# Optimization experiments

Hardware: AMD Instinct MI355X
Metric: run time of the kernel (lower is better)

Reference implementation:

```python
import jax, jax.numpy as jnp
import numpy as np

B, S, D, H = 2, 2048, 1024, 16
DK = D // H

def setup_inputs() -> dict:
    key = jax.random.key(0)
    ks = jax.random.split(key, 11)
    scale = 0.02
    inp = {
        "Q": jax.random.normal(ks[0], (B, S, D), jnp.float32),
        "K": jax.random.normal(ks[1], (B, S, D), jnp.float32),
        "V": jax.random.normal(ks[2], (B, S, D), jnp.float32),
        "mask": jnp.ones((B, S), jnp.int32),
        "Wq": jax.random.normal(ks[3], (D, D), jnp.float32) * scale,
        "bq": jnp.zeros((D,), jnp.float32),
        "Wk": jax.random.normal(ks[4], (D, D), jnp.float32) * scale,
        "bk": jnp.zeros((D,), jnp.float32),
        "Wv": jax.random.normal(ks[5], (D, D), jnp.float32) * scale,
        "bv": jnp.zeros((D,), jnp.float32),
        "Wo": jax.random.normal(ks[6], (D, D), jnp.float32) * scale,
        "bo": jnp.zeros((D,), jnp.float32),
    }
    return inp

def _split_heads(x):
    # [B,S,D] -> [B,H,S,DK]
    return x.reshape(B, S, H, DK).transpose(0, 2, 1, 3)

def reference(Q, K, V, mask, Wq, bq, Wk, bk, Wv, bv, Wo, bo):
    q = _split_heads(Q @ Wq.T + bq)
    k = _split_heads(K @ Wk.T + bk)
    v = _split_heads(V @ Wv.T + bv)
    scores = jnp.einsum("bhqd,bhkd->bhqk", q, k) / jnp.sqrt(jnp.float32(DK))
    # 2D padding mask -> [B,1,1,S], mask==0 positions set to -inf
    m = mask[:, None, None, :]
    scores = jnp.where(m == 0, -jnp.inf, scores)
    attn_weights = jax.nn.softmax(scores, axis=-1)  # [B,H,S,S]
    attn_output = jnp.einsum("bhqk,bhkd->bhqd", attn_weights, v)
    attn_output = attn_output.transpose(0, 2, 1, 3).reshape(B, S, D)
    output = attn_output @ Wo.T + bo
    return (output, attn_weights)
```

## Files before the change

### kernel.cpp

```cpp
#include <hip/hip_runtime.h>
#include <stdint.h>

#define DEVINL __device__ __forceinline__

typedef float  f32x4  __attribute__((ext_vector_type(4)));
typedef float  f32x16 __attribute__((ext_vector_type(16)));
typedef short  s16x8  __attribute__((ext_vector_type(8)));
typedef unsigned short u16x4 __attribute__((ext_vector_type(4)));
typedef unsigned short u16x8 __attribute__((ext_vector_type(8)));

static constexpr int S = 2048, D = 1024, H = 16;
static constexpr size_t OUT0 = (size_t)2 * S * D;

DEVINL unsigned short f2bf(float f) {
  union { float f; unsigned u; } v; v.f = f;
  unsigned r = v.u + 0x7FFFu + ((v.u >> 16) & 1u);
  return (unsigned short)(r >> 16);
}

DEVINL unsigned cvt_pk_bf16(float lo, float hi) {
  unsigned r;
  asm("v_cvt_pk_bf16_f32 %0, %1, %2" : "=v"(r) : "v"(lo), "v"(hi));
  return r;
}

DEVINL void perm32swap(unsigned& a, unsigned& b) {
#if __has_builtin(__builtin_amdgcn_permlane32_swap)
  auto r = __builtin_amdgcn_permlane32_swap(a, b, false, false);
  a = r[0]; b = r[1];
#else
  asm volatile("v_permlane32_swap_b32 %0, %1" : "+v"(a), "+v"(b));
#endif
}

DEVINL void gload_lds16(const void* g, void* l) {
  __builtin_amdgcn_global_load_lds(
      (const __attribute__((address_space(1))) unsigned int*)g,
      (__attribute__((address_space(3))) unsigned int*)l, 16, 0, 0);
}

DEVINL void cvt_body(const float* __restrict__ src, unsigned short* __restrict__ dst, int i) {
  const f32x4* s4 = (const f32x4*)src;
  f32x4 a = s4[i * 2], b = s4[i * 2 + 1];
  u16x8 o;
  o[0] = f2bf(a[0]); o[1] = f2bf(a[1]); o[2] = f2bf(a[2]); o[3] = f2bf(a[3]);
  o[4] = f2bf(b[0]); o[5] = f2bf(b[1]); o[6] = f2bf(b[2]); o[7] = f2bf(b[3]);
  ((u16x8*)dst)[i] = o;
}

__global__ __launch_bounds__(256) void k_cvt_all(
    const float* __restrict__ Q, const float* __restrict__ K, const float* __restrict__ V,
    const float* __restrict__ Wq, const float* __restrict__ Wk,
    const float* __restrict__ Wv, const float* __restrict__ Wo,
    unsigned short* __restrict__ Xq, unsigned short* __restrict__ Xk,
    unsigned short* __restrict__ Xv,
    unsigned short* __restrict__ WQ, unsigned short* __restrict__ WK,
    unsigned short* __restrict__ WV, unsigned short* __restrict__ WO) {
  int i = blockIdx.x;
  const float* src; unsigned short* dst; int item;
  if (i < 6144) {
    int z = i >> 11;
    item = (i & 2047) * 256 + threadIdx.x;
    src = z == 0 ? Q : z == 1 ? K : V;
    dst = z == 0 ? Xq : z == 1 ? Xk : Xv;
  } else {
    int j = i - 6144, z = j >> 9;
    item = (j & 511) * 256 + threadIdx.x;
    src = z == 0 ? Wq : z == 1 ? Wk : z == 2 ? Wv : Wo;
    dst = z == 0 ? WQ : z == 1 ? WK : z == 2 ? WV : WO;
  }
  cvt_body(src, dst, item);
}

template <int MODE>
DEVINL void gemm_tile(const unsigned short* __restrict__ A,
                      const unsigned short* __restrict__ Bw,
                      const float* __restrict__ bias, void* __restrict__ Cout,
                      int tileM, int tileN, float scl, char* smem) {
  unsigned short* As = (unsigned short*)smem;
  unsigned short* Bs = (unsigned short*)(smem + 8192);
  const int tid = threadIdx.x;
  const int lane = tid & 63, wave = tid >> 6;
  const int wr = wave >> 1, wc = wave & 1;
  const int l15 = lane & 15, l16 = lane >> 4;
  f32x4 acc[4][4] = {};
  for (int k0 = 0; k0 < 1024; k0 += 32) {
#pragma unroll
    for (int p = 0; p < 2; ++p) {
      int c = tid + p * 256;
      int row = c >> 2, col = (c & 3) * 8;
      gload_lds16(A + (((size_t)(tileM + row)) << 10) + k0 + col, &As[c * 8]);
      gload_lds16(Bw + (((size_t)(tileN + row)) << 10) + k0 + col, &Bs[c * 8]);
    }
    __syncthreads();
    s16x8 af[4], bf[4];
#pragma unroll
    for (int i = 0; i < 4; ++i)
      af[i] = *(const s16x8*)&As[(wr * 64 + i * 16 + l15) * 32 + l16 * 8];
#pragma unroll
    for (int i = 0; i < 4; ++i)
      bf[i] = *(const s16x8*)&Bs[(wc * 64 + i * 16 + l15) * 32 + l16 * 8];
#pragma unroll
    for (int i = 0; i < 4; ++i)
#pragma unroll
      for (int j = 0; j < 4; ++j)
        acc[i][j] = __builtin_amdgcn_mfma_f32_16x16x32_bf16(af[i], bf[j], acc[i][j], 0, 0, 0);
    __syncthreads();
  }

  if (MODE == 2) {
    unsigned short* T = (unsigned short*)smem;
#pragma unroll
    for (int i = 0; i < 4; ++i)
#pragma unroll
      for (int j = 0; j < 4; ++j) {
        int n = wc * 64 + j * 16 + l15;
        float bv = bias[tileN + n];
        int m0 = wr * 64 + i * 16 + l16 * 4;
        u16x4 o;
#pragma unroll
        for (int r = 0; r < 4; ++r) o[r] = f2bf(acc[i][j][r] + bv);
        *(u16x4*)((char*)T + n * 256 + ((m0 * 2) ^ ((n & 15) << 4))) = o;
      }
    __syncthreads();
    {
      int n = tid >> 1, mh = tid & 1;
      int d = (tileN + n) & 63, h_ = (tileN + n) >> 6;
      int b_ = tileM >> 11;
      int kt_ = (((tileM & 2047) + mh * 64) >> 6);
      unsigned short* dst = (unsigned short*)Cout + (size_t)(b_ * H + h_) * S * 64 +
                            (size_t)kt_ * 4096 + d * 64;
#pragma unroll
      for (int k = 0; k < 8; ++k) {
        int mc = mh * 64 + k * 8;
        u16x8 v = *(const u16x8*)((const char*)T + n * 256 + ((mc * 2) ^ ((n & 15) << 4)));
        *(u16x8*)(dst + k * 8) = v;
      }
    }
  } else {
#pragma unroll
    for (int i = 0; i < 4; ++i) {
#pragma unroll
      for (int j = 0; j < 4; ++j) {
        int n = tileN + wc * 64 + j * 16 + l15;
        float bv = bias[n];
#pragma unroll
        for (int r = 0; r < 4; ++r) {
          int m = tileM + wr * 64 + i * 16 + l16 * 4 + r;
          float v = (acc[i][j][r] + bv) * scl;
          if (MODE == 0) {
            int b_ = m >> 11, s_ = m & 2047, h_ = n >> 6, d_ = n & 63;
            ((unsigned short*)Cout)[(((size_t)(b_ * H + h_) * S) + s_) * 64 + d_] = f2bf(v);
          } else {
            ((float*)Cout)[(size_t)m * 1024 + n] = v;
          }
        }
      }
    }
  }
}

__global__ __launch_bounds__(256) void k_gemm_qkv(
    const unsigned short* __restrict__ Xq, const unsigned short* __restrict__ Xk,
    const unsigned short* __restrict__ Xv,
    const unsigned short* __restrict__ Wq, const unsigned short* __restrict__ Wk,
    const unsigned short* __restrict__ Wv,
    const float* __restrict__ bq, const float* __restrict__ bk, const float* __restrict__ bv,
    unsigned short* __restrict__ oq, unsigned short* __restrict__ ok,
    unsigned short* __restrict__ vt2) {
  __shared__ alignas(16) char smem[32768];
  int flat = (blockIdx.z * 32 + blockIdx.y) * 8 + blockIdx.x;
  int swz = (flat & 7) * 96 + (flat >> 3);
  int z = swz >> 8;
  int rem = swz & 255;
  int ty = rem >> 3, tx = rem & 7;
  if (z == 2) {
    gemm_tile<2>(Xv, Wv, bv, vt2, ty * 128, tx * 128, 1.0f, smem);
  } else {
    const unsigned short* A = z == 0 ? Xq : Xk;
    const unsigned short* W = z == 0 ? Wq : Wk;
    const float* bias = z == 0 ? bq : bk;
    unsigned short* o = z == 0 ? oq : ok;
    gemm_tile<0>(A, W, bias, o, ty * 128, tx * 128, z == 0 ? 0.125f : 1.0f, smem);
  }
}

__global__ __launch_bounds__(256) void k_gemm_out(const unsigned short* __restrict__ A,
                                                  const unsigned short* __restrict__ W,
                                                  const float* __restrict__ bias,
                                                  float* __restrict__ Cout) {
  __shared__ alignas(16) char smem[16384];
  int flat = blockIdx.y * 8 + blockIdx.x;
  int swz = (flat & 7) * 32 + (flat >> 3);
  int ty = swz >> 3, tx = swz & 7;
  gemm_tile<1>(A, W, bias, Cout, ty * 128, tx * 128, 1.0f, smem);
}

__global__ __launch_bounds__(256) void k_attn_fused(const unsigned short* __restrict__ qw,
                                                    const unsigned short* __restrict__ kw,
                                                    const unsigned short* __restrict__ vt2,
                                                    const int* __restrict__ mask,
                                                    unsigned short* __restrict__ aout,
                                                    float* __restrict__ attw) {
  __shared__ alignas(16) char lds[33536];
  unsigned short* Ks = (unsigned short*)lds;
  unsigned short* Vs = (unsigned short*)(lds + 16384);
  float* lsumW = (float*)(lds + 32768);
  float* lsumT = (float*)(lds + 33280);
  float* nl2lW = (float*)(lds + 33408);
  const float LOG2E = 1.44269504f;

  int flat = blockIdx.y * 64 + blockIdx.x;
  int swzb = (flat & 7) * 256 + (flat >> 3);
  const int bh = swzb >> 6, b = bh >> 4, h = bh & 15;
  const int q0 = (swzb & 63) * 32;
  const int tid = threadIdx.x;
  const int lane = tid & 63, w = tid >> 6;
  const int l31 = lane & 31, hi = lane >> 5;

  const unsigned short* kw_bh = kw + (size_t)bh * S * 64;
  const unsigned short* vt_bh = vt2 + (size_t)bh * S * 64;
  const int* mrow = mask + b * S;

  s16x8 qf[4];
  const unsigned short* qbase = qw + ((size_t)bh * S + q0 + l31) * 64 + hi * 8;
#pragma unroll
  for (int kc = 0; kc < 4; ++kc) qf[kc] = *(const s16x8*)(qbase + kc * 16);

  f32x16 oT0 = {}, oT1 = {};
  float lsum = 0.f;
  const int swv = (l31 & 15) << 4;

  for (int t = 0; t < 16; ++t) {
#pragma unroll
    for (int p = 0; p < 4; ++p) {
      int c = tid + p * 256, row = c >> 3, cc = (c & 7) ^ (row & 7);
      gload_lds16(kw_bh + ((size_t)(t * 128 + row)) * 64 + cc * 8, Ks + c * 8);
    }
#pragma unroll
    for (int p = 0; p < 4; ++p) {
      int c = tid + p * 256, row = c >> 4, c16 = (c & 15) ^ (row & 15);
      gload_lds16(vt_bh + (size_t)(t * 2 + (c16 >> 3)) * 4096 + row * 64 + (c16 & 7) * 8,
                  Vs + c * 8);
    }
    __syncthreads();

    const int krow = w * 32 + l31;
    f32x16 sT = {};
#pragma unroll
    for (int kc = 0; kc < 4; ++kc) {
      s16x8 ka = *(const s16x8*)((const char*)Ks + krow * 128 +
                                 ((kc * 32 + hi * 16) ^ ((krow & 7) << 4)));
      sT = __builtin_amdgcn_mfma_f32_32x32x16_bf16(ka, qf[kc], sT, 0, 0, 0);
    }

    int base = t * 128 + w * 32 + 4 * hi;
    int m[16];
    *(int4*)&m[0]  = *(const int4*)&mrow[base];
    *(int4*)&m[4]  = *(const int4*)&mrow[base + 8];
    *(int4*)&m[8]  = *(const int4*)&mrow[base + 16];
    *(int4*)&m[12] = *(const int4*)&mrow[base + 24];

    float e[16];
#pragma unroll
    for (int r = 0; r < 16; ++r) {
      e[r] = m[r] ? exp2f(sT[r] * LOG2E) : 0.f;
      lsum += e[r];
    }

    unsigned x0 = cvt_pk_bf16(e[0], e[1]),   x1 = cvt_pk_bf16(e[2], e[3]);
    unsigned x2 = cvt_pk_bf16(e[4], e[5]),   x3 = cvt_pk_bf16(e[6], e[7]);
    unsigned x4 = cvt_pk_bf16(e[8], e[9]),   x5 = cvt_pk_bf16(e[10], e[11]);
    unsigned x6 = cvt_pk_bf16(e[12], e[13]), x7 = cvt_pk_bf16(e[14], e[15]);
    perm32swap(x0, x2); perm32swap(x1, x3);
    perm32swap(x4, x6); perm32swap(x5, x7);
    union { unsigned u[4]; s16x8 v; } p0u, p1u;
    p0u.u[0] = x0; p0u.u[1] = x1; p0u.u[2] = x2; p0u.u[3] = x3;
    p1u.u[0] = x4; p1u.u[1] = x5; p1u.u[2] = x6; p1u.u[3] = x7;

    const int ko0 = w * 64 + hi * 16, ko1 = w * 64 + 32 + hi * 16;
    const char* Vr0 = (const char*)Vs + l31 * 256;
    const char* Vr1 = (const char*)Vs + (32 + l31) * 256;
    s16x8 va;
    va = *(const s16x8*)(Vr0 + (ko0 ^ swv));
    oT0 = __builtin_amdgcn_mfma_f32_32x32x16_bf16(va, p0u.v, oT0, 0, 0, 0);
    va = *(const s16x8*)(Vr0 + (ko1 ^ swv));
    oT0 = __builtin_amdgcn_mfma_f32_32x32x16_bf16(va, p1u.v, oT0, 0, 0, 0);
    va = *(const s16x8*)(Vr1 + (ko0 ^ swv));
    oT1 = __builtin_amdgcn_mfma_f32_32x32x16_bf16(va, p0u.v, oT1, 0, 0, 0);
    va = *(const s16x8*)(Vr1 + (ko1 ^ swv));
    oT1 = __builtin_amdgcn_mfma_f32_32x32x16_bf16(va, p1u.v, oT1, 0, 0, 0);

    __syncthreads();
  }

  lsum += __shfl_xor(lsum, 32);
  if (hi == 0) lsumW[w * 32 + l31] = lsum;

  {
    char* orow = (char*)lds + w * 8192 + l31 * 256;
#pragma unroll
    for (int rg = 0; rg < 4; ++rg) {
      f32x4 c0, c1;
#pragma unroll
      for (int j = 0; j < 4; ++j) { c0[j] = oT0[rg * 4 + j]; c1[j] = oT1[rg * 4 + j]; }
      *(f32x4*)(orow + ((rg * 32 + hi * 16) ^ swv)) = c0;
      *(f32x4*)(orow + ((128 + rg * 32 + hi * 16) ^ swv)) = c1;
    }
  }
  __syncthreads();

  if (tid < 32) {
    float tot = lsumW[tid] + lsumW[32 + tid] + lsumW[64 + tid] + lsumW[96 + tid];
    lsumT[tid] = tot;
    nl2lW[tid] = __log2f(tot);
  }
  __syncthreads();

  {
    int q = tid >> 3, dg = tid & 7;
    float inv = 1.f / lsumT[q];
    int sq = (q & 15) << 4;
    float s[8] = {};
#pragma unroll
    for (int w4 = 0; w4 < 4; ++w4) {
      const char* prow = (const char*)lds + w4 * 8192 + q * 256;
      f32x4 a = *(const f32x4*)(prow + ((dg * 32) ^ sq));
      f32x4 bb = *(const f32x4*)(prow + ((dg * 32 + 16) ^ sq));
#pragma unroll
      for (int j = 0; j < 4; ++j) { s[j] += a[j]; s[4 + j] += bb[j]; }
    }
    u16x8 ob;
#pragma unroll
    for (int j = 0; j < 8; ++j) ob[j] = f2bf(s[j] * inv);
    *(u16x8*)&aout[((size_t)b * S + q0 + q) * D + h * 64 + dg * 8] = ob;
  }

  float nl2l[16];
#pragma unroll
  for (int r = 0; r < 16; ++r) nl2l[r] = nl2lW[(r & 3) + 8 * (r >> 2) + 4 * hi];

  for (int it = 0; it < 16; ++it) {
    int key0 = it * 128 + w * 32;
    const unsigned short* kbase = kw_bh + (size_t)(key0 + l31) * 64 + hi * 8;
    s16x8 kb[4];
#pragma unroll
    for (int kc = 0; kc < 4; ++kc) kb[kc] = *(const s16x8*)(kbase + kc * 16);
    f32x16 dacc = {};
#pragma unroll
    for (int kc = 0; kc < 4; ++kc)
      dacc = __builtin_amdgcn_mfma_f32_32x32x16_bf16(qf[kc], kb[kc], dacc, 0, 0, 0);

    int key = key0 + l31;
    int mk = mrow[key];
    float* obase = attw + ((size_t)bh * S + q0) * S + key;
#pragma unroll
    for (int r = 0; r < 16; ++r) {
      int row = (r & 3) + 8 * (r >> 2) + 4 * hi;
      float wv = mk ? exp2f(dacc[r] * LOG2E - nl2l[r]) : 0.f;
      __builtin_nontemporal_store(wv, obase + (size_t)row * S);
    }
  }
}

extern "C" void kernel_launch(void* const* d_in, const int* in_sizes, int n_in,
                              void* d_out, int out_size, void* d_ws, size_t ws_size,
                              hipStream_t stream) {
  (void)in_sizes; (void)n_in; (void)out_size; (void)ws_size;
  const float* Q  = (const float*)d_in[0];
  const float* K  = (const float*)d_in[1];
  const float* V  = (const float*)d_in[2];
  const int* mask = (const int*)d_in[3];
  const float* Wq = (const float*)d_in[4];
  const float* bq = (const float*)d_in[5];
  const float* Wk = (const float*)d_in[6];
  const float* bk = (const float*)d_in[7];
  const float* Wv = (const float*)d_in[8];
  const float* bv = (const float*)d_in[9];
  const float* Wo = (const float*)d_in[10];
  const float* bo = (const float*)d_in[11];

  char* ws = (char*)d_ws;
  unsigned short* Xbf  = (unsigned short*)(ws + 0);
  unsigned short* Wbf  = (unsigned short*)(ws + 25165824);
  unsigned short* qws  = (unsigned short*)(ws + 33554432);
  unsigned short* kws  = (unsigned short*)(ws + 41943040);
  unsigned short* vt2  = (unsigned short*)(ws + 50331648);
  unsigned short* aoutb= (unsigned short*)(ws + 8388608);
  float* out0 = (float*)d_out;
  float* attw = (float*)d_out + OUT0;

  k_cvt_all<<<dim3(8192), dim3(256), 0, stream>>>(
      Q, K, V, Wq, Wk, Wv, Wo,
      Xbf, Xbf + 4194304, Xbf + 8388608,
      Wbf, Wbf + 1048576, Wbf + 2097152, Wbf + 3145728);

  k_gemm_qkv<<<dim3(8, 32, 3), dim3(256), 0, stream>>>(
      Xbf, Xbf + 4194304, Xbf + 8388608,
      Wbf, Wbf + 1048576, Wbf + 2097152,
      bq, bk, bv, qws, kws, vt2);

  k_attn_fused<<<dim3(64, 32), dim3(256), 0, stream>>>(qws, kws, vt2, mask, aoutb, attw);

  k_gemm_out<<<dim3(8, 32), dim3(256), 0, stream>>>(aoutb, Wbf + 3145728, bo, out0);
}
```

Baseline: 241.7 us.

## Double-buffer K/V tiles and process 64 queries per attention block

The attention kernel now handles 64 queries per block (two query groups of two waves each, each wave covering 32 keys) instead of 32 queries with four waves over 128 keys. K and V tiles of 64 keys are double-buffered in LDS so the next tile's global-to-LDS load is issued before computing on the current one, removing one barrier-exposed load stall per iteration. Each K/V tile is reused by twice as many queries, halving K/V traffic per query, but the grid is halved to 1024 blocks and the reduction/epilogue indexing is rewritten.

```diff
diff --git a/kernel.cpp b/kernel.cpp
--- a/kernel.cpp
+++ b/kernel.cpp
@@ -202,59 +202,67 @@
                                                     const int* __restrict__ mask,
                                                     unsigned short* __restrict__ aout,
                                                     float* __restrict__ attw) {
-  __shared__ alignas(16) char lds[33536];
-  unsigned short* Ks = (unsigned short*)lds;
-  unsigned short* Vs = (unsigned short*)(lds + 16384);
+  __shared__ alignas(16) char lds[33792];
   float* lsumW = (float*)(lds + 32768);
   float* lsumT = (float*)(lds + 33280);
-  float* nl2lW = (float*)(lds + 33408);
+  float* nl2lW = (float*)(lds + 33536);
   const float LOG2E = 1.44269504f;
 
-  int flat = blockIdx.y * 64 + blockIdx.x;
-  int swzb = (flat & 7) * 256 + (flat >> 3);
-  const int bh = swzb >> 6, b = bh >> 4, h = bh & 15;
-  const int q0 = (swzb & 63) * 32;
+  int flat = blockIdx.y * 32 + blockIdx.x;
+  int swzb = (flat & 7) * 128 + (flat >> 3);
+  const int bh = swzb >> 5, b = bh >> 4, h = bh & 15;
+  const int q0 = (swzb & 31) * 64;
   const int tid = threadIdx.x;
   const int lane = tid & 63, w = tid >> 6;
   const int l31 = lane & 31, hi = lane >> 5;
+  const int qg = w >> 1, kb = w & 1;
 
   const unsigned short* kw_bh = kw + (size_t)bh * S * 64;
   const unsigned short* vt_bh = vt2 + (size_t)bh * S * 64;
   const int* mrow = mask + b * S;
 
   s16x8 qf[4];
-  const unsigned short* qbase = qw + ((size_t)bh * S + q0 + l31) * 64 + hi * 8;
+  const unsigned short* qbase = qw + ((size_t)bh * S + q0 + qg * 32 + l31) * 64 + hi * 8;
 #pragma unroll
   for (int kc = 0; kc < 4; ++kc) qf[kc] = *(const s16x8*)(qbase + kc * 16);
 
   f32x16 oT0 = {}, oT1 = {};
   float lsum = 0.f;
-  const int swv = (l31 & 15) << 4;
-
-  for (int t = 0; t < 16; ++t) {
-#pragma unroll
-    for (int p = 0; p < 4; ++p) {
-      int c = tid + p * 256, row = c >> 3, cc = (c & 7) ^ (row & 7);
-      gload_lds16(kw_bh + ((size_t)(t * 128 + row)) * 64 + cc * 8, Ks + c * 8);
-    }
-#pragma unroll
-    for (int p = 0; p < 4; ++p) {
-      int c = tid + p * 256, row = c >> 4, c16 = (c & 15) ^ (row & 15);
-      gload_lds16(vt_bh + (size_t)(t * 2 + (c16 >> 3)) * 4096 + row * 64 + (c16 & 7) * 8,
-                  Vs + c * 8);
-    }
-    __syncthreads();
-
-    const int krow = w * 32 + l31;
+  const int swv = (l31 & 7) << 4;
+
+#pragma unroll
+  for (int p = 0; p < 2; ++p) {
+    int c = tid + p * 256, row = c >> 3, cc = (c & 7) ^ (row & 7);
+    gload_lds16(kw_bh + (size_t)row * 64 + cc * 8, lds + c * 16);
+    gload_lds16(vt_bh + (size_t)row * 64 + cc * 8, lds + 16384 + c * 16);
+  }
+  __syncthreads();
+
+  int cur = 0;
+  for (int t = 0; t < 32; ++t) {
+    if (t + 1 < 32) {
+      int nt = t + 1;
+      int nxt = (cur ^ 1) * 8192;
+#pragma unroll
+      for (int p = 0; p < 2; ++p) {
+        int c = tid + p * 256, row = c >> 3, cc = (c & 7) ^ (row & 7);
+        gload_lds16(kw_bh + ((size_t)(nt * 64 + row)) * 64 + cc * 8, lds + nxt + c * 16);
+        gload_lds16(vt_bh + (size_t)nt * 4096 + row * 64 + cc * 8, lds + 16384 + nxt + c * 16);
+      }
+    }
+    const char* Kc = lds + cur * 8192;
+    const char* Vc = lds + 16384 + cur * 8192;
+
+    const int krow = kb * 32 + l31;
     f32x16 sT = {};
 #pragma unroll
     for (int kc = 0; kc < 4; ++kc) {
-      s16x8 ka = *(const s16x8*)((const char*)Ks + krow * 128 +
+      s16x8 ka = *(const s16x8*)(Kc + krow * 128 +
                                  ((kc * 32 + hi * 16) ^ ((krow & 7) << 4)));
       sT = __builtin_amdgcn_mfma_f32_32x32x16_bf16(ka, qf[kc], sT, 0, 0, 0);
     }
 
-    int base = t * 128 + w * 32 + 4 * hi;
+    int base = t * 64 + kb * 32 + 4 * hi;
     int m[16];
     *(int4*)&m[0]  = *(const int4*)&mrow[base];
     *(int4*)&m[4]  = *(const int4*)&mrow[base + 8];
@@ -278,9 +286,9 @@
     p0u.u[0] = x0; p0u.u[1] = x1; p0u.u[2] = x2; p0u.u[3] = x3;
     p1u.u[0] = x4; p1u.u[1] = x5; p1u.u[2] = x6; p1u.u[3] = x7;
 
-    const int ko0 = w * 64 + hi * 16, ko1 = w * 64 + 32 + hi * 16;
-    const char* Vr0 = (const char*)Vs + l31 * 256;
-    const char* Vr1 = (const char*)Vs + (32 + l31) * 256;
+    const int ko0 = kb * 64 + hi * 16, ko1 = kb * 64 + 32 + hi * 16;
+    const char* Vr0 = Vc + l31 * 128;
+    const char* Vr1 = Vc + (32 + l31) * 128;
     s16x8 va;
     va = *(const s16x8*)(Vr0 + (ko0 ^ swv));
     oT0 = __builtin_amdgcn_mfma_f32_32x32x16_bf16(va, p0u.v, oT0, 0, 0, 0);
@@ -292,68 +300,76 @@
     oT1 = __builtin_amdgcn_mfma_f32_32x32x16_bf16(va, p1u.v, oT1, 0, 0, 0);
 
     __syncthreads();
+    cur ^= 1;
   }
 
   lsum += __shfl_xor(lsum, 32);
   if (hi == 0) lsumW[w * 32 + l31] = lsum;
 
+  const int sqq = (l31 & 15) << 4;
   {
-    char* orow = (char*)lds + w * 8192 + l31 * 256;
+    char* orow = lds + w * 8192 + l31 * 256;
 #pragma unroll
     for (int rg = 0; rg < 4; ++rg) {
       f32x4 c0, c1;
 #pragma unroll
       for (int j = 0; j < 4; ++j) { c0[j] = oT0[rg * 4 + j]; c1[j] = oT1[rg * 4 + j]; }
-      *(f32x4*)(orow + ((rg * 32 + hi * 16) ^ swv)) = c0;
-      *(f32x4*)(orow + ((128 + rg * 32 + hi * 16) ^ swv)) = c1;
+      *(f32x4*)(orow + ((rg * 32 + hi * 16) ^ sqq)) = c0;
+      *(f32x4*)(orow + ((128 + rg * 32 + hi * 16) ^ sqq)) = c1;
     }
   }
   __syncthreads();
 
-  if (tid < 32) {
-    float tot = lsumW[tid] + lsumW[32 + tid] + lsumW[64 + tid] + lsumW[96 + tid];
+  if (tid < 64) {
+    int qg_ = tid >> 5, qq = tid & 31;
+    float tot = lsumW[qg_ * 64 + qq] + lsumW[qg_ * 64 + 32 + qq];
     lsumT[tid] = tot;
     nl2lW[tid] = __log2f(tot);
   }
   __syncthreads();
 
   {
-    int q = tid >> 3, dg = tid & 7;
+    int q = tid >> 2, dq = tid & 3;
+    int qg_ = q >> 5, qq = q & 31;
     float inv = 1.f / lsumT[q];
-    int sq = (q & 15) << 4;
-    float s[8] = {};
-#pragma unroll
-    for (int w4 = 0; w4 < 4; ++w4) {
-      const char* prow = (const char*)lds + w4 * 8192 + q * 256;
-      f32x4 a = *(const f32x4*)(prow + ((dg * 32) ^ sq));
-      f32x4 bb = *(const f32x4*)(prow + ((dg * 32 + 16) ^ sq));
-#pragma unroll
-      for (int j = 0; j < 4; ++j) { s[j] += a[j]; s[4 + j] += bb[j]; }
-    }
-    u16x8 ob;
-#pragma unroll
-    for (int j = 0; j < 8; ++j) ob[j] = f2bf(s[j] * inv);
-    *(u16x8*)&aout[((size_t)b * S + q0 + q) * D + h * 64 + dg * 8] = ob;
+    int sq = (qq & 15) << 4;
+    float s[16] = {};
+#pragma unroll
+    for (int w2 = 0; w2 < 2; ++w2) {
+      const char* prow = lds + (qg_ * 2 + w2) * 8192 + qq * 256;
+#pragma unroll
+      for (int c = 0; c < 4; ++c) {
+        f32x4 a = *(const f32x4*)(prow + ((dq * 64 + c * 16) ^ sq));
+#pragma unroll
+        for (int j = 0; j < 4; ++j) s[c * 4 + j] += a[j];
+      }
+    }
+    u16x8 ob0, ob1;
+#pragma unroll
+    for (int j = 0; j < 8; ++j) { ob0[j] = f2bf(s[j] * inv); ob1[j] = f2bf(s[8 + j] * inv); }
+    unsigned short* abase = aout + ((size_t)b * S + q0 + q) * D + h * 64 + dq * 16;
+    *(u16x8*)abase = ob0;
+    *(u16x8*)(abase + 8) = ob1;
   }
 
   float nl2l[16];
 #pragma unroll
-  for (int r = 0; r < 16; ++r) nl2l[r] = nl2lW[(r & 3) + 8 * (r >> 2) + 4 * hi];
-
-  for (int it = 0; it < 16; ++it) {
-    int key0 = it * 128 + w * 32;
+  for (int r = 0; r < 16; ++r) nl2l[r] = nl2lW[qg * 32 + (r & 3) + 8 * (r >> 2) + 4 * hi];
+
+  for (int it = 0; it < 32; ++it) {
+    int key0 = it * 64 + kb * 32;
     const unsigned short* kbase = kw_bh + (size_t)(key0 + l31) * 64 + hi * 8;
-    s16x8 kb[4];
-#pragma unroll
-    for (int kc = 0; kc < 4; ++kc) kb[kc] = *(const s16x8*)(kbase + kc * 16);
+    s16x8 kfr[4];
+#pragma unroll
+    for (int kc = 0; kc < 4; ++kc) kfr[kc] = *(const s16x8*)(kbase + kc * 16);
     f32x16 dacc = {};
 #pragma unroll
     for (int kc = 0; kc < 4; ++kc)
-      dacc = __builtin_amdgcn_mfma_f32_32x32x16_bf16(qf[kc], kb[kc], dacc, 0, 0, 0);
+      dacc = __builtin_amdgcn_mfma_f32_32x32x16_bf16(qf[kc], kfr[kc], dacc, 0, 0, 0);
 
     int key = key0 + l31;
     int mk = mrow[key];
-    float* obase = attw + ((size_t)bh * S + q0) * S + key;
+    float* obase = attw + ((size_t)bh * S + q0 + qg * 32) * S + key;
 #pragma unroll
     for (int r = 0; r < 16; ++r) {
       int row = (r & 3) + 8 * (r >> 2) + 4 * hi;
@@ -400,7 +416,7 @@
       Wbf, Wbf + 1048576, Wbf + 2097152,
       bq, bk, bv, qws, kws, vt2);
 
-  k_attn_fused<<<dim3(64, 32), dim3(256), 0, stream>>>(qws, kws, vt2, mask, aoutb, attw);
+  k_attn_fused<<<dim3(32, 32), dim3(256), 0, stream>>>(qws, kws, vt2, mask, aoutb, attw);
 
   k_gemm_out<<<dim3(8, 32), dim3(256), 0, stream>>>(aoutb, Wbf + 3145728, bo, out0);
 }
```

Result: faster. 234.5 us (-3.0%).
